# Optimization experiments

Measured on AMD Instinct MI355X. Metric: run time of the kernel, lower is better.

Reference implementation:

```python
import jax, jax.numpy as jnp
import numpy as np

B, C, H, W, T = 2, 96, 64, 64, 64
NH = 8  # num_heads
WS = 2  # window size per axis (2,2,2)


def setup_inputs() -> dict:
    key = jax.random.key(0)
    ks = jax.random.split(key, 9)
    s = lambda fan_in: 1.0 / np.sqrt(fan_in)
    return {
        "x": jax.random.normal(ks[0], (B, C, H, W, T), dtype=jnp.float32),
        # linear weights stored [in, out] (transposed vs torch nn.Linear)
        "qkv_w": jax.random.normal(ks[1], (C, 3 * C), dtype=jnp.float32) * s(C),
        "qkv_b": jax.random.normal(ks[2], (3 * C,), dtype=jnp.float32) * 0.01,
        "merge_w": jax.random.normal(ks[3], (C, C), dtype=jnp.float32) * s(C),
        "merge_b": jax.random.normal(ks[4], (C,), dtype=jnp.float32) * 0.01,
        "w1": jax.random.normal(ks[5], (2 * C, C), dtype=jnp.float32) * s(2 * C),
        "b1": jax.random.normal(ks[6], (C,), dtype=jnp.float32) * 0.01,
        "w2": jax.random.normal(ks[7], (C, C), dtype=jnp.float32) * s(C),
        "b2": jax.random.normal(ks[8], (C,), dtype=jnp.float32) * 0.01,
    }


def reference(x, qkv_w, qkv_b, merge_w, merge_b, w1, b1, w2, b2):
    b, c, h, w, t = x.shape
    hd = c // NH
    scale = hd ** -0.5
    n = WS * WS * WS  # 8 tokens per window

    xp = jnp.transpose(x, (0, 2, 3, 4, 1))  # [B,H,W,T,C]
    # window partition -> [B*nWin, 8, C]
    xw = xp.reshape(b, h // WS, WS, w // WS, WS, t // WS, WS, c)
    xw = jnp.transpose(xw, (0, 1, 3, 5, 2, 4, 6, 7)).reshape(-1, n, c)

    # windowed MHSA
    qkv = (xw @ qkv_w + qkv_b).reshape(-1, n, 3, NH, hd)
    q, k, v = jnp.moveaxis(qkv, 2, 0)  # each [Bw, n, NH, hd]
    attn = jax.nn.softmax(jnp.einsum('bnhd,bmhd->bhnm', q * scale, k), axis=-1)
    msg = jnp.einsum('bhnm,bmhd->bnhd', attn, v).reshape(-1, n, c)
    msg = msg @ merge_w + merge_b

    # window reverse -> [B,H,W,T,C]
    msg = msg.reshape(b, h // WS, w // WS, t // WS, WS, WS, WS, c)
    msg = jnp.transpose(msg, (0, 1, 4, 2, 5, 3, 6, 7)).reshape(b, h, w, t, c)

    # concat residual path + MLP (GELU exact, matching torch nn.GELU default)
    xt = xp.reshape(b, h * w * t, c)
    mt = msg.reshape(b, h * w * t, c)
    hmid = jax.nn.gelu(jnp.concatenate([xt, mt], axis=-1) @ w1 + b1, approximate=False)
    out = hmid @ w2 + b2
    return jnp.transpose(out.reshape(b, h, w, t, c), (0, 4, 1, 2, 3))
```

## Files before the change

### kernel.cpp

```cpp
#include <hip/hip_runtime.h>
#include <math.h>

typedef short bf16x8 __attribute__((ext_vector_type(8)));
typedef float f32x4 __attribute__((ext_vector_type(4)));

__device__ __forceinline__ ushort f2bf(float f) {
  union { float f; unsigned int i; } v; v.f = f;
  unsigned int x = v.i;
  return (ushort)((x + 0x7fffu + ((x >> 16) & 1u)) >> 16);
}
__device__ __forceinline__ float bf2f(ushort u) {
  union { unsigned int i; float f; } v; v.i = ((unsigned int)u) << 16; return v.f;
}
__device__ __forceinline__ float bfLo(unsigned int d) {
  union { unsigned int i; float f; } v; v.i = d << 16; return v.f;
}
__device__ __forceinline__ float bfHi(unsigned int d) {
  union { unsigned int i; float f; } v; v.i = d & 0xffff0000u; return v.f;
}

__global__ void swizzle_w(const float* __restrict__ qkv_w,
                          const float* __restrict__ merge_w,
                          const float* __restrict__ w1,
                          const float* __restrict__ w2,
                          ushort* __restrict__ ws) {
  int g = blockIdx.x * 256 + threadIdx.x;
  if (g >= 8064) return;
  int tile = g >> 6, lane = g & 63;
  const float* src; int ld, c0, k0, rem;
  if (tile < 54)       { rem = tile % 18; src = qkv_w;   ld = 288; c0 = (tile / 18) * 96 + (rem / 3) * 16; k0 = (rem % 3) * 32; }
  else if (tile < 72)  { rem = tile - 54; src = merge_w; ld = 96;  c0 = (rem / 3) * 16; k0 = (rem % 3) * 32; }
  else if (tile < 90)  { rem = tile - 72; src = w1;      ld = 96;  c0 = (rem / 3) * 16; k0 = (rem % 3) * 32; }
  else if (tile < 108) { rem = tile - 90; src = w1;      ld = 96;  c0 = (rem / 3) * 16; k0 = 96 + (rem % 3) * 32; }
  else                 { rem = tile - 108; src = w2;     ld = 96;  c0 = (rem / 3) * 16; k0 = (rem % 3) * 32; }
  int n = c0 + (lane & 15);
  int kb = k0 + (lane >> 4) * 8;
  ushort tmp[8];
#pragma unroll
  for (int j = 0; j < 8; ++j) tmp[j] = f2bf(src[(size_t)(kb + j) * ld + n]);
  *(uint4*)(ws + tile * 512 + lane * 8) = *(const uint4*)tmp;
}

#define KPAD 104
#define QPAD 68
#define OPAD 65
__global__ __launch_bounds__(256, 3) void swin_mfma(
    const float* __restrict__ x,
    const float* __restrict__ qkv_b, const float* __restrict__ merge_b,
    const float* __restrict__ b1, const float* __restrict__ b2,
    const ushort* __restrict__ wsw, float* __restrict__ out) {
  __shared__ __align__(16) ushort R[288 * QPAD];

  const int tid = threadIdx.x, bid = blockIdx.x;
  const int t0 = bid & 3, w0 = (bid >> 2) & 31, h0 = (bid >> 7) & 31, b = bid >> 12;
  const int lane = tid & 63, wave = tid >> 6;
  const int mrow = lane & 15, quad = lane >> 4;
  const int arow = (wave * 16 + mrow) * KPAD + quad * 8;
  const int tokb = wave * 16 + quad * 4;

  for (int i = tid; i < 1536; i += 256) {
    int q = i & 3, dw = (i >> 2) & 1, dh = (i >> 3) & 1, c = i >> 4;
    size_t g = ((((size_t)b * 96 + c) * 64 + h0 * 2 + dh) * 64 + w0 * 2 + dw) * 64 + t0 * 16 + q * 4;
    float4 v = *(const float4*)(x + g);
    float vv[4] = {v.x, v.y, v.z, v.w};
    int base = dh * 4 + dw * 2;
#pragma unroll
    for (int j = 0; j < 4; ++j) {
      int tl = q * 4 + j;
      R[((tl >> 1) * 8 + base + (tl & 1)) * KPAD + c] = f2bf(vv[j]);
    }
  }
  __syncthreads();

  bf16x8 aX[3];
#pragma unroll
  for (int kt = 0; kt < 3; ++kt)
    aX[kt] = *(const bf16x8*)(R + arow + kt * 32);
  __syncthreads();

  for (int cn = 0; cn < 3; ++cn) {
#pragma unroll
    for (int nt = 0; nt < 6; ++nt) {
      int col = cn * 96 + nt * 16 + mrow;
      float bias = qkv_b[col];
      f32x4 acc = {bias, bias, bias, bias};
#pragma unroll
      for (int kt = 0; kt < 3; ++kt) {
        bf16x8 bf = *(const bf16x8*)(wsw + (size_t)(cn * 18 + nt * 3 + kt) * 512 + lane * 8);
        acc = __builtin_amdgcn_mfma_f32_16x16x32_bf16(aX[kt], bf, acc, 0, 0, 0);
      }
#pragma unroll
      for (int r = 0; r < 4; ++r) R[col * QPAD + tokb + r] = f2bf(acc[r]);
    }
  }
  __syncthreads();

  {
    const int win = tid >> 5, head = (tid >> 2) & 7, r2 = (tid & 3) * 2;
    const ushort* Qb = R + (head * 12) * QPAD + win * 8;
    const ushort* Kb = R + (96 + head * 12) * QPAD + win * 8;
    const ushort* Vb = R + (192 + head * 12) * QPAD + win * 8;
    const float scale = 0.28867513459481287f;
    float q0[12], q1[12];
#pragma unroll
    for (int d = 0; d < 12; ++d) {
      unsigned int qq = *(const unsigned int*)(Qb + d * QPAD + r2);
      q0[d] = bfLo(qq) * scale;
      q1[d] = bfHi(qq) * scale;
    }
    float s0[8] = {0, 0, 0, 0, 0, 0, 0, 0}, s1[8] = {0, 0, 0, 0, 0, 0, 0, 0};
#pragma unroll
    for (int d = 0; d < 12; ++d) {
      uint2 ka = *(const uint2*)(Kb + d * QPAD);
      uint2 kc = *(const uint2*)(Kb + d * QPAD + 4);
      float kf[8] = {bfLo(ka.x), bfHi(ka.x), bfLo(ka.y), bfHi(ka.y),
                     bfLo(kc.x), bfHi(kc.x), bfLo(kc.y), bfHi(kc.y)};
#pragma unroll
      for (int m = 0; m < 8; ++m) { s0[m] += q0[d] * kf[m]; s1[m] += q1[d] * kf[m]; }
    }
    float mx0 = fmaxf(fmaxf(fmaxf(s0[0], s0[1]), fmaxf(s0[2], s0[3])),
                      fmaxf(fmaxf(s0[4], s0[5]), fmaxf(s0[6], s0[7])));
    float mx1 = fmaxf(fmaxf(fmaxf(s1[0], s1[1]), fmaxf(s1[2], s1[3])),
                      fmaxf(fmaxf(s1[4], s1[5]), fmaxf(s1[6], s1[7])));
    float sum0 = 0.f, sum1 = 0.f;
#pragma unroll
    for (int m = 0; m < 8; ++m) {
      s0[m] = __expf(s0[m] - mx0); sum0 += s0[m];
      s1[m] = __expf(s1[m] - mx1); sum1 += s1[m];
    }
    float inv0 = 1.0f / sum0, inv1 = 1.0f / sum1;
    float o0[12], o1[12];
#pragma unroll
    for (int d = 0; d < 12; ++d) {
      uint2 va = *(const uint2*)(Vb + d * QPAD);
      uint2 vc = *(const uint2*)(Vb + d * QPAD + 4);
      float vf[8] = {bfLo(va.x), bfHi(va.x), bfLo(va.y), bfHi(va.y),
                     bfLo(vc.x), bfHi(vc.x), bfLo(vc.y), bfHi(vc.y)};
      float a0 = 0.f, a1 = 0.f;
#pragma unroll
      for (int m = 0; m < 8; ++m) { a0 += s0[m] * vf[m]; a1 += s1[m] * vf[m]; }
      o0[d] = a0 * inv0; o1[d] = a1 * inv1;
    }
    __syncthreads();
    int tr = win * 8 + r2;
#pragma unroll
    for (int d = 0; d < 12; ++d) {
      R[tr * KPAD + head * 12 + d] = f2bf(o0[d]);
      R[(tr + 1) * KPAD + head * 12 + d] = f2bf(o1[d]);
    }
  }
  __syncthreads();

  {
    bf16x8 aM[3];
#pragma unroll
    for (int kt = 0; kt < 3; ++kt) aM[kt] = *(const bf16x8*)(R + arow + kt * 32);
#pragma unroll
    for (int nt = 0; nt < 6; ++nt) {
      int col = nt * 16 + mrow;
      float bias = merge_b[col];
      f32x4 acc = {bias, bias, bias, bias};
#pragma unroll
      for (int kt = 0; kt < 3; ++kt) {
        bf16x8 bf = *(const bf16x8*)(wsw + (size_t)(54 + nt * 3 + kt) * 512 + lane * 8);
        acc = __builtin_amdgcn_mfma_f32_16x16x32_bf16(aM[kt], bf, acc, 0, 0, 0);
      }
#pragma unroll
      for (int r = 0; r < 4; ++r) R[(tokb + r) * KPAD + col] = f2bf(acc[r]);
    }
  }
  __syncthreads();

  {
    bf16x8 aM2[3];
#pragma unroll
    for (int kt = 0; kt < 3; ++kt) aM2[kt] = *(const bf16x8*)(R + arow + kt * 32);
#pragma unroll
    for (int nt = 0; nt < 6; ++nt) {
      int col = nt * 16 + mrow;
      float bias = b1[col];
      f32x4 acc = {bias, bias, bias, bias};
#pragma unroll
      for (int kt = 0; kt < 3; ++kt) {
        bf16x8 bf = *(const bf16x8*)(wsw + (size_t)(72 + nt * 3 + kt) * 512 + lane * 8);
        acc = __builtin_amdgcn_mfma_f32_16x16x32_bf16(aX[kt], bf, acc, 0, 0, 0);
      }
#pragma unroll
      for (int kt = 0; kt < 3; ++kt) {
        bf16x8 bf = *(const bf16x8*)(wsw + (size_t)(90 + nt * 3 + kt) * 512 + lane * 8);
        acc = __builtin_amdgcn_mfma_f32_16x16x32_bf16(aM2[kt], bf, acc, 0, 0, 0);
      }
#pragma unroll
      for (int r = 0; r < 4; ++r) {
        float h = acc[r];
        float gel = 0.5f * h * (1.0f + erff(h * 0.70710678118654752f));
        R[6656 + (tokb + r) * KPAD + col] = f2bf(gel);
      }
    }
  }
  __syncthreads();

  {
    bf16x8 aH[3];
#pragma unroll
    for (int kt = 0; kt < 3; ++kt) aH[kt] = *(const bf16x8*)(R + 6656 + arow + kt * 32);
#pragma unroll
    for (int nt = 0; nt < 6; ++nt) {
      int col = nt * 16 + mrow;
      float bias = b2[col];
      f32x4 acc = {bias, bias, bias, bias};
#pragma unroll
      for (int kt = 0; kt < 3; ++kt) {
        bf16x8 bf = *(const bf16x8*)(wsw + (size_t)(108 + nt * 3 + kt) * 512 + lane * 8);
        acc = __builtin_amdgcn_mfma_f32_16x16x32_bf16(aH[kt], bf, acc, 0, 0, 0);
      }
#pragma unroll
      for (int r = 0; r < 4; ++r) R[col * OPAD + tokb + r] = f2bf(acc[r]);
    }
  }
  __syncthreads();

  for (int i = tid; i < 1536; i += 256) {
    int q = i & 3, dw = (i >> 2) & 1, dh = (i >> 3) & 1, c = i >> 4;
    float vv[4];
#pragma unroll
    for (int j = 0; j < 4; ++j) {
      int tl = q * 4 + j;
      vv[j] = bf2f(R[c * OPAD + (tl >> 1) * 8 + dh * 4 + dw * 2 + (tl & 1)]);
    }
    float4 v = {vv[0], vv[1], vv[2], vv[3]};
    size_t g = ((((size_t)b * 96 + c) * 64 + h0 * 2 + dh) * 64 + w0 * 2 + dw) * 64 + t0 * 16 + q * 4;
    *(float4*)(out + g) = v;
  }
}

extern "C" void kernel_launch(void* const* d_in, const int* in_sizes, int n_in,
                              void* d_out, int out_size, void* d_ws, size_t ws_size,
                              hipStream_t stream) {
  const float* x = (const float*)d_in[0];
  const float* qkv_w = (const float*)d_in[1];
  const float* qkv_b = (const float*)d_in[2];
  const float* merge_w = (const float*)d_in[3];
  const float* merge_b = (const float*)d_in[4];
  const float* w1 = (const float*)d_in[5];
  const float* b1 = (const float*)d_in[6];
  const float* w2 = (const float*)d_in[7];
  const float* b2 = (const float*)d_in[8];
  ushort* wsw = (ushort*)d_ws;
  swizzle_w<<<dim3(32), dim3(256), 0, stream>>>(qkv_w, merge_w, w1, w2, wsw);
  swin_mfma<<<dim3(8192), dim3(256), 0, stream>>>(
      x, qkv_b, merge_b, b1, b2, wsw, (float*)d_out);
}
```

Baseline: 556.2 us.

## Fold merge projection into first MLP weight and fold attention scale into Q

Precomputes merge_w @ w1[96:] and merge_b @ w1[96:] + b1 in the weight-prep kernel, so the per-block merge GEMM, its LDS write-back and one barrier disappear; the MLP first layer now consumes the attention output directly. The softmax scale is folded into the Q weights and Q bias, removing per-element multiplies in attention. This adds a small serial dot-product loop to the prep kernel and changes bf16 rounding points slightly.

```diff
diff --git a/kernel.cpp b/kernel.cpp
--- a/kernel.cpp
+++ b/kernel.cpp
@@ -3,6 +3,8 @@
 
 typedef short bf16x8 __attribute__((ext_vector_type(8)));
 typedef float f32x4 __attribute__((ext_vector_type(4)));
+
+#define SCALE_Q 0.28867513459481287f
 
 __device__ __forceinline__ ushort f2bf(float f) {
   union { float f; unsigned int i; } v; v.f = f;
@@ -21,24 +23,57 @@
 
 __global__ void swizzle_w(const float* __restrict__ qkv_w,
                           const float* __restrict__ merge_w,
+                          const float* __restrict__ merge_b,
                           const float* __restrict__ w1,
+                          const float* __restrict__ b1,
                           const float* __restrict__ w2,
                           ushort* __restrict__ ws) {
   int g = blockIdx.x * 256 + threadIdx.x;
-  if (g >= 8064) return;
-  int tile = g >> 6, lane = g & 63;
-  const float* src; int ld, c0, k0, rem;
-  if (tile < 54)       { rem = tile % 18; src = qkv_w;   ld = 288; c0 = (tile / 18) * 96 + (rem / 3) * 16; k0 = (rem % 3) * 32; }
-  else if (tile < 72)  { rem = tile - 54; src = merge_w; ld = 96;  c0 = (rem / 3) * 16; k0 = (rem % 3) * 32; }
-  else if (tile < 90)  { rem = tile - 72; src = w1;      ld = 96;  c0 = (rem / 3) * 16; k0 = (rem % 3) * 32; }
-  else if (tile < 108) { rem = tile - 90; src = w1;      ld = 96;  c0 = (rem / 3) * 16; k0 = 96 + (rem % 3) * 32; }
-  else                 { rem = tile - 108; src = w2;     ld = 96;  c0 = (rem / 3) * 16; k0 = (rem % 3) * 32; }
-  int n = c0 + (lane & 15);
-  int kb = k0 + (lane >> 4) * 8;
-  ushort tmp[8];
-#pragma unroll
-  for (int j = 0; j < 8; ++j) tmp[j] = f2bf(src[(size_t)(kb + j) * ld + n]);
-  *(uint4*)(ws + tile * 512 + lane * 8) = *(const uint4*)tmp;
+  if (g < 6912) {
+    int tile = g >> 6, lane = g & 63;
+    float vals[8];
+    if (tile < 54) {
+      int rem = tile % 18;
+      int c0 = (tile / 18) * 96 + (rem / 3) * 16, k0 = (rem % 3) * 32;
+      int n = c0 + (lane & 15), kb = k0 + (lane >> 4) * 8;
+      float s = (tile < 18) ? SCALE_Q : 1.0f;
+#pragma unroll
+      for (int j = 0; j < 8; ++j) vals[j] = qkv_w[(size_t)(kb + j) * 288 + n] * s;
+    } else if (tile < 72) {
+      int rem = tile - 54;
+      int c0 = (rem / 3) * 16, k0 = (rem % 3) * 32;
+      int n = c0 + (lane & 15), kb = k0 + (lane >> 4) * 8;
+#pragma unroll
+      for (int j = 0; j < 8; ++j) vals[j] = w1[(size_t)(kb + j) * 96 + n];
+    } else if (tile < 90) {
+      int rem = tile - 72;
+      int c0 = (rem / 3) * 16, k0 = (rem % 3) * 32;
+      int n = c0 + (lane & 15), kb = k0 + (lane >> 4) * 8;
+      float acc[8] = {0, 0, 0, 0, 0, 0, 0, 0};
+      for (int m = 0; m < 96; ++m) {
+        float wr = w1[(size_t)(96 + m) * 96 + n];
+#pragma unroll
+        for (int j = 0; j < 8; ++j) acc[j] += merge_w[(size_t)(kb + j) * 96 + m] * wr;
+      }
+#pragma unroll
+      for (int j = 0; j < 8; ++j) vals[j] = acc[j];
+    } else {
+      int rem = tile - 90;
+      int c0 = (rem / 3) * 16, k0 = (rem % 3) * 32;
+      int n = c0 + (lane & 15), kb = k0 + (lane >> 4) * 8;
+#pragma unroll
+      for (int j = 0; j < 8; ++j) vals[j] = w2[(size_t)(kb + j) * 96 + n];
+    }
+    ushort tmp[8];
+#pragma unroll
+    for (int j = 0; j < 8; ++j) tmp[j] = f2bf(vals[j]);
+    *(uint4*)(ws + tile * 512 + lane * 8) = *(const uint4*)tmp;
+  } else if (g < 7008) {
+    int n = g - 6912;
+    float s = b1[n];
+    for (int m = 0; m < 96; ++m) s += merge_b[m] * w1[(size_t)(96 + m) * 96 + n];
+    ((float*)(ws + 55296))[n] = s;
+  }
 }
 
 #define KPAD 104
@@ -46,8 +81,7 @@
 #define OPAD 65
 __global__ __launch_bounds__(256, 3) void swin_mfma(
     const float* __restrict__ x,
-    const float* __restrict__ qkv_b, const float* __restrict__ merge_b,
-    const float* __restrict__ b1, const float* __restrict__ b2,
+    const float* __restrict__ qkv_b, const float* __restrict__ b2,
     const ushort* __restrict__ wsw, float* __restrict__ out) {
   __shared__ __align__(16) ushort R[288 * QPAD];
 
@@ -57,6 +91,7 @@
   const int mrow = lane & 15, quad = lane >> 4;
   const int arow = (wave * 16 + mrow) * KPAD + quad * 8;
   const int tokb = wave * 16 + quad * 4;
+  const float* foldb = (const float*)(wsw + 55296);
 
   for (int i = tid; i < 1536; i += 256) {
     int q = i & 3, dw = (i >> 2) & 1, dh = (i >> 3) & 1, c = i >> 4;
@@ -83,6 +118,7 @@
     for (int nt = 0; nt < 6; ++nt) {
       int col = cn * 96 + nt * 16 + mrow;
       float bias = qkv_b[col];
+      if (cn == 0) bias *= SCALE_Q;
       f32x4 acc = {bias, bias, bias, bias};
 #pragma unroll
       for (int kt = 0; kt < 3; ++kt) {
@@ -100,13 +136,12 @@
     const ushort* Qb = R + (head * 12) * QPAD + win * 8;
     const ushort* Kb = R + (96 + head * 12) * QPAD + win * 8;
     const ushort* Vb = R + (192 + head * 12) * QPAD + win * 8;
-    const float scale = 0.28867513459481287f;
     float q0[12], q1[12];
 #pragma unroll
     for (int d = 0; d < 12; ++d) {
       unsigned int qq = *(const unsigned int*)(Qb + d * QPAD + r2);
-      q0[d] = bfLo(qq) * scale;
-      q1[d] = bfHi(qq) * scale;
+      q0[d] = bfLo(qq);
+      q1[d] = bfHi(qq);
     }
     float s0[8] = {0, 0, 0, 0, 0, 0, 0, 0}, s1[8] = {0, 0, 0, 0, 0, 0, 0, 0};
 #pragma unroll
@@ -152,42 +187,22 @@
   __syncthreads();
 
   {
-    bf16x8 aM[3];
-#pragma unroll
-    for (int kt = 0; kt < 3; ++kt) aM[kt] = *(const bf16x8*)(R + arow + kt * 32);
+    bf16x8 aM2[3];
+#pragma unroll
+    for (int kt = 0; kt < 3; ++kt) aM2[kt] = *(const bf16x8*)(R + arow + kt * 32);
 #pragma unroll
     for (int nt = 0; nt < 6; ++nt) {
       int col = nt * 16 + mrow;
-      float bias = merge_b[col];
+      float bias = foldb[col];
       f32x4 acc = {bias, bias, bias, bias};
 #pragma unroll
       for (int kt = 0; kt < 3; ++kt) {
         bf16x8 bf = *(const bf16x8*)(wsw + (size_t)(54 + nt * 3 + kt) * 512 + lane * 8);
-        acc = __builtin_amdgcn_mfma_f32_16x16x32_bf16(aM[kt], bf, acc, 0, 0, 0);
-      }
-#pragma unroll
-      for (int r = 0; r < 4; ++r) R[(tokb + r) * KPAD + col] = f2bf(acc[r]);
-    }
-  }
-  __syncthreads();
-
-  {
-    bf16x8 aM2[3];
-#pragma unroll
-    for (int kt = 0; kt < 3; ++kt) aM2[kt] = *(const bf16x8*)(R + arow + kt * 32);
-#pragma unroll
-    for (int nt = 0; nt < 6; ++nt) {
-      int col = nt * 16 + mrow;
-      float bias = b1[col];
-      f32x4 acc = {bias, bias, bias, bias};
+        acc = __builtin_amdgcn_mfma_f32_16x16x32_bf16(aX[kt], bf, acc, 0, 0, 0);
+      }
 #pragma unroll
       for (int kt = 0; kt < 3; ++kt) {
         bf16x8 bf = *(const bf16x8*)(wsw + (size_t)(72 + nt * 3 + kt) * 512 + lane * 8);
-        acc = __builtin_amdgcn_mfma_f32_16x16x32_bf16(aX[kt], bf, acc, 0, 0, 0);
-      }
-#pragma unroll
-      for (int kt = 0; kt < 3; ++kt) {
-        bf16x8 bf = *(const bf16x8*)(wsw + (size_t)(90 + nt * 3 + kt) * 512 + lane * 8);
         acc = __builtin_amdgcn_mfma_f32_16x16x32_bf16(aM2[kt], bf, acc, 0, 0, 0);
       }
 #pragma unroll
@@ -211,7 +226,7 @@
       f32x4 acc = {bias, bias, bias, bias};
 #pragma unroll
       for (int kt = 0; kt < 3; ++kt) {
-        bf16x8 bf = *(const bf16x8*)(wsw + (size_t)(108 + nt * 3 + kt) * 512 + lane * 8);
+        bf16x8 bf = *(const bf16x8*)(wsw + (size_t)(90 + nt * 3 + kt) * 512 + lane * 8);
         acc = __builtin_amdgcn_mfma_f32_16x16x32_bf16(aH[kt], bf, acc, 0, 0, 0);
       }
 #pragma unroll
@@ -247,7 +262,7 @@
   const float* w2 = (const float*)d_in[7];
   const float* b2 = (const float*)d_in[8];
   ushort* wsw = (ushort*)d_ws;
-  swizzle_w<<<dim3(32), dim3(256), 0, stream>>>(qkv_w, merge_w, w1, w2, wsw);
+  swizzle_w<<<dim3(28), dim3(256), 0, stream>>>(qkv_w, merge_w, merge_b, w1, b1, w2, wsw);
   swin_mfma<<<dim3(8192), dim3(256), 0, stream>>>(
-      x, qkv_b, merge_b, b1, b2, wsw, (float*)d_out);
-}
+      x, qkv_b, b2, wsw, (float*)d_out);
+}
```

After: 553.3 us. About the same (-0.5%).
